# Kernel tuning notes

Measured on AMD Instinct MI355X. Metric: run time of the kernel, lower is better.

The kernel has to match this reference:

```python
import jax, jax.numpy as jnp
import numpy as np

N = 100000      # nodes
E = 3200000     # edges (avg degree 32)
F_IN = 512
F_OUT = 256


def setup_inputs() -> dict:
    key = jax.random.key(0)
    k1, k2, k3, k4, k5, k6 = jax.random.split(key, 6)
    x = jax.random.normal(k1, (N, F_IN), dtype=jnp.float32)
    row = jax.random.randint(k2, (E,), 0, N)            # destination node of each edge
    col = jax.random.randint(k3, (E,), 0, N)            # source node of each edge
    edge_val = jax.random.uniform(k4, (E,), dtype=jnp.float32)  # normalized adj weights
    stdv = 1.0 / np.sqrt(F_OUT)                         # matches reset_parameters()
    weight = jax.random.uniform(k5, (F_IN, F_OUT), dtype=jnp.float32, minval=-stdv, maxval=stdv)
    bias = jax.random.uniform(k6, (F_OUT,), dtype=jnp.float32, minval=-stdv, maxval=stdv)
    return {"input": x, "weight": weight, "bias": bias, "edge_val": edge_val, "row": row, "col": col}


def reference(input, weight, bias, edge_val, row, col):
    # support = X @ W  (dense projection)
    support = input @ weight                             # [N, F_OUT]
    # SpMM: out[r] += a[r,c] * support[c] over COO edges (torch.spmm(adj, support))
    msgs = edge_val[:, None] * support[col]              # [E, F_OUT] gather + scale
    agg = jax.ops.segment_sum(msgs, row, num_segments=input.shape[0])  # scatter-add
    # np.around(..., decimals=3) applied row-wise in the original
    out = jnp.round(agg * 1000.0) / 1000.0
    return out + bias
```

## Files before the change

### kernel.cpp

```cpp
#include <hip/hip_runtime.h>
#include <hip/hip_bf16.h>

#define N_NODES 100000
#define N_EDGES 3200000
#define FIN 512
#define FOUT 256
#define GEMM_BM 128
#define GEMM_BK 32

#define NP 782
#define CAP_LDS 4608
#define SC_CHUNK 16384

typedef __attribute__((ext_vector_type(8))) short short8;
typedef __attribute__((ext_vector_type(4))) float f32x4;

__device__ __forceinline__ unsigned short f2bf(float f) {
    unsigned u = __float_as_uint(f);
    u += 0x7fffu + ((u >> 16) & 1u);
    return (unsigned short)(u >> 16);
}
__device__ __forceinline__ float bf2f(unsigned short h) {
    return __uint_as_float(((unsigned)h) << 16);
}

__global__ __launch_bounds__(256) void prep_weight(const float* __restrict__ W,
                                                   unsigned short* __restrict__ Wt) {
    int idx = blockIdx.x * 256 + threadIdx.x;
    if (idx < FIN * FOUT) {
        int k = idx >> 8;
        int n = idx & 255;
        Wt[(size_t)(k >> 5) * (FOUT * GEMM_BK) + n * GEMM_BK + (k & 31)] = f2bf(W[idx]);
    }
}

__global__ __launch_bounds__(512, 4)
void gemm_kernel(const float* __restrict__ X, const unsigned short* __restrict__ Wt,
                 unsigned short* __restrict__ support) {
    __shared__ unsigned short A_lds[GEMM_BM][40];
    __shared__ unsigned short B_lds[FOUT][40];

    const int t = threadIdx.x;
    const int lane = t & 63;
    const int w = t >> 6;
    const int wm = w >> 2;
    const int wn = w & 3;
    const int q = lane >> 4;
    const int lr = lane & 15;
    const int m0 = blockIdx.x * GEMM_BM;

    f32x4 acc[4][4];
#pragma unroll
    for (int i = 0; i < 4; i++)
#pragma unroll
        for (int j = 0; j < 4; j++) acc[i][j] = (f32x4)0.0f;

    const int arow = t >> 2;
    const int acol = (t & 3) * 8;
    const bool avalid = (m0 + arow) < N_NODES;
    const float* Xp = X + (size_t)(m0 + arow) * FIN + acol;

    const int brow = t >> 1;
    const int bcol = (t & 1) * 16;

    for (int s = 0; s < FIN / GEMM_BK; ++s) {
        union { __hip_bfloat162 h[4]; uint4 v; } pk;
        if (avalid) {
            float4 v0 = *(const float4*)(Xp + s * GEMM_BK);
            float4 v1 = *(const float4*)(Xp + s * GEMM_BK + 4);
            pk.h[0] = __float22bfloat162_rn(make_float2(v0.x, v0.y));
            pk.h[1] = __float22bfloat162_rn(make_float2(v0.z, v0.w));
            pk.h[2] = __float22bfloat162_rn(make_float2(v1.x, v1.y));
            pk.h[3] = __float22bfloat162_rn(make_float2(v1.z, v1.w));
        } else {
            pk.v = make_uint4(0, 0, 0, 0);
        }
        const uint4* bsrc = (const uint4*)(Wt + (size_t)s * (FOUT * GEMM_BK) + brow * GEMM_BK + bcol);
        uint4 b0 = bsrc[0], b1 = bsrc[1];

        __syncthreads();
        *(uint4*)&A_lds[arow][acol] = pk.v;
        *(uint4*)&B_lds[brow][bcol] = b0;
        *(uint4*)&B_lds[brow][bcol + 8] = b1;
        __syncthreads();

        short8 af[4], bfr[4];
#pragma unroll
        for (int i = 0; i < 4; i++) af[i] = *(const short8*)&A_lds[wm * 64 + i * 16 + lr][q * 8];
#pragma unroll
        for (int j = 0; j < 4; j++) bfr[j] = *(const short8*)&B_lds[wn * 64 + j * 16 + lr][q * 8];
#pragma unroll
        for (int i = 0; i < 4; i++)
#pragma unroll
            for (int j = 0; j < 4; j++)
                acc[i][j] = __builtin_amdgcn_mfma_f32_16x16x32_bf16(af[i], bfr[j], acc[i][j], 0, 0, 0);
    }

#pragma unroll
    for (int i = 0; i < 4; i++) {
#pragma unroll
        for (int r = 0; r < 4; r++) {
            int gm = m0 + wm * 64 + i * 16 + q * 4 + r;
            if (gm < N_NODES) {
#pragma unroll
                for (int j = 0; j < 4; j++)
                    support[(size_t)gm * FOUT + wn * 64 + j * 16 + lr] = f2bf(acc[i][j][r]);
            }
        }
    }
}

__global__ __launch_bounds__(256) void part_hist(const int* __restrict__ row,
                                                 unsigned* __restrict__ pcnt) {
    __shared__ unsigned bins[NP];
    for (int i = threadIdx.x; i < NP; i += 256) bins[i] = 0;
    __syncthreads();
    const int e0 = blockIdx.x * 8192;
#pragma unroll
    for (int j = 0; j < 32; ++j) {
        int e = e0 + j * 256 + threadIdx.x;
        if (e < N_EDGES) atomicAdd(&bins[((unsigned)row[e]) >> 7], 1u);
    }
    __syncthreads();
    for (int i = threadIdx.x; i < NP; i += 256)
        if (bins[i]) atomicAdd(&pcnt[i], bins[i]);
}

__global__ __launch_bounds__(1024) void part_scan(const unsigned* __restrict__ pcnt,
                                                  unsigned* __restrict__ base,
                                                  unsigned* __restrict__ cursor,
                                                  unsigned* __restrict__ row_ptr) {
    __shared__ unsigned s[1024];
    const int t = threadIdx.x;
    unsigned v = (t < NP) ? pcnt[t] : 0u;
    s[t] = v;
    __syncthreads();
#pragma unroll
    for (int off = 1; off < 1024; off <<= 1) {
        unsigned tv = (t >= off) ? s[t - off] : 0u;
        __syncthreads();
        s[t] += tv;
        __syncthreads();
    }
    if (t < NP) {
        unsigned b = s[t] - v;
        base[t] = b;
        cursor[t] = b;
    }
    if (t == 0) {
        base[NP] = N_EDGES;
        row_ptr[N_NODES] = N_EDGES;
    }
}

__global__ __launch_bounds__(256) void part_scatter(const int* __restrict__ row,
                                                    const int* __restrict__ col,
                                                    const float* __restrict__ val,
                                                    unsigned* __restrict__ cursor,
                                                    uint2* __restrict__ part) {
    __shared__ unsigned bins[NP];
    __shared__ unsigned gb[NP];
    for (int i = threadIdx.x; i < NP; i += 256) bins[i] = 0;
    __syncthreads();
    const int e0 = blockIdx.x * SC_CHUNK;
#pragma unroll 4
    for (int j = 0; j < SC_CHUNK / 256; ++j) {
        int e = e0 + j * 256 + threadIdx.x;
        if (e < N_EDGES) atomicAdd(&bins[((unsigned)row[e]) >> 7], 1u);
    }
    __syncthreads();
    for (int i = threadIdx.x; i < NP; i += 256) {
        unsigned c = bins[i];
        gb[i] = c ? atomicAdd(&cursor[i], c) : 0u;
        bins[i] = 0;
    }
    __syncthreads();
#pragma unroll 4
    for (int j = 0; j < SC_CHUNK / 256; ++j) {
        int e = e0 + j * 256 + threadIdx.x;
        if (e < N_EDGES) {
            unsigned r = (unsigned)row[e];
            unsigned p = r >> 7;
            unsigned l = atomicAdd(&bins[p], 1u);
            part[gb[p] + l] = make_uint2(((unsigned)col[e]) | ((r & 127u) << 17),
                                         __float_as_uint(val[e]));
        }
    }
}

__global__ __launch_bounds__(256) void part_finalize(const unsigned* __restrict__ base,
                                                     uint2* __restrict__ part,
                                                     unsigned* __restrict__ row_ptr) {
    __shared__ uint2 recs[CAP_LDS];
    __shared__ unsigned ncnt[128], nsc[128], ccur[128];
    const int p = blockIdx.x;
    const int t = threadIdx.x;
    const unsigned b = base[p];
    unsigned cnt = base[p + 1] - b;
    if (cnt > CAP_LDS) cnt = CAP_LDS;
    if (t < 128) ncnt[t] = 0;
    __syncthreads();
    for (unsigned i = t; i < cnt; i += 256) {
        uint2 r = part[b + i];
        recs[i] = r;
        atomicAdd(&ncnt[r.x >> 17], 1u);
    }
    __syncthreads();
    if (t < 128) nsc[t] = ncnt[t];
    __syncthreads();
#pragma unroll
    for (int off = 1; off < 128; off <<= 1) {
        unsigned tv = (t < 128 && t >= off) ? nsc[t - off] : 0u;
        __syncthreads();
        if (t < 128) nsc[t] += tv;
        __syncthreads();
    }
    if (t < 128) {
        unsigned ex = nsc[t] - ncnt[t];
        ccur[t] = ex;
        int node = p * 128 + t;
        if (node < N_NODES) row_ptr[node] = b + ex;
    }
    __syncthreads();
    for (unsigned i = t; i < cnt; i += 256) {
        uint2 r = recs[i];
        unsigned pos = atomicAdd(&ccur[r.x >> 17], 1u);
        part[b + pos] = make_uint2(r.x & 0x1FFFFu, r.y);
    }
}

__global__ __launch_bounds__(256)
void spmm_kernel(const unsigned* __restrict__ row_ptr, const uint2* __restrict__ sorted,
                 const unsigned short* __restrict__ support, const float* __restrict__ bias,
                 float* __restrict__ out) {
    const int lane = threadIdx.x & 63;
    const int n = blockIdx.x * 4 + (threadIdx.x >> 6);
    const unsigned start = __builtin_amdgcn_readfirstlane(row_ptr[n]);
    const unsigned end   = __builtin_amdgcn_readfirstlane(row_ptr[n + 1]);
    const int fo = lane * 4;
    const unsigned short* sp = support + fo;
    float a0 = 0.f, a1 = 0.f, a2 = 0.f, a3 = 0.f;

    unsigned i = start;
    const unsigned nfull = (end - start) >> 3;
    if (nfull) {
        uint2 e[8];
#pragma unroll
        for (int j = 0; j < 8; ++j) e[j] = sorted[i + j];
        for (unsigned bt = 1; bt < nfull; ++bt) {
            ushort4 s[8];
#pragma unroll
            for (int j = 0; j < 8; ++j) s[j] = *(const ushort4*)(sp + (size_t)e[j].x * FOUT);
            uint2 en[8];
#pragma unroll
            for (int j = 0; j < 8; ++j) en[j] = sorted[i + 8 + j];
#pragma unroll
            for (int j = 0; j < 8; ++j) {
                float v = __uint_as_float(e[j].y);
                a0 += v * bf2f(s[j].x); a1 += v * bf2f(s[j].y);
                a2 += v * bf2f(s[j].z); a3 += v * bf2f(s[j].w);
            }
#pragma unroll
            for (int j = 0; j < 8; ++j) e[j] = en[j];
            i += 8;
        }
        ushort4 s[8];
#pragma unroll
        for (int j = 0; j < 8; ++j) s[j] = *(const ushort4*)(sp + (size_t)e[j].x * FOUT);
#pragma unroll
        for (int j = 0; j < 8; ++j) {
            float v = __uint_as_float(e[j].y);
            a0 += v * bf2f(s[j].x); a1 += v * bf2f(s[j].y);
            a2 += v * bf2f(s[j].z); a3 += v * bf2f(s[j].w);
        }
        i += 8;
    }
    for (; i < end; ++i) {
        uint2 e = sorted[i];
        float v = __uint_as_float(e.y);
        ushort4 s0 = *(const ushort4*)(sp + (size_t)e.x * FOUT);
        a0 += v * bf2f(s0.x); a1 += v * bf2f(s0.y); a2 += v * bf2f(s0.z); a3 += v * bf2f(s0.w);
    }

    float4 bv = *(const float4*)(bias + fo);
    float4 r;
    r.x = rintf(a0 * 1000.f) * 0.001f + bv.x;
    r.y = rintf(a1 * 1000.f) * 0.001f + bv.y;
    r.z = rintf(a2 * 1000.f) * 0.001f + bv.z;
    r.w = rintf(a3 * 1000.f) * 0.001f + bv.w;
    *(float4*)(out + (size_t)n * FOUT + fo) = r;
}

extern "C" void kernel_launch(void* const* d_in, const int* in_sizes, int n_in,
                              void* d_out, int out_size, void* d_ws, size_t ws_size,
                              hipStream_t stream) {
    (void)in_sizes; (void)n_in; (void)out_size; (void)ws_size;
    const float* X    = (const float*)d_in[0];
    const float* W    = (const float*)d_in[1];
    const float* bias = (const float*)d_in[2];
    const float* eval = (const float*)d_in[3];
    const int*   row  = (const int*)d_in[4];
    const int*   col  = (const int*)d_in[5];
    float* out = (float*)d_out;

    char* p = (char*)d_ws;
    auto take = [&](size_t bytes) {
        char* r = p;
        p += (bytes + 511) & ~(size_t)511;
        return r;
    };
    unsigned short* support = (unsigned short*)take((size_t)N_NODES * FOUT * 2);
    unsigned short* Wt      = (unsigned short*)take((size_t)FIN * FOUT * 2);
    unsigned*       pcnt    = (unsigned*)take((size_t)NP * 4);
    unsigned*       base    = (unsigned*)take((size_t)(NP + 1) * 4);
    unsigned*       cursor  = (unsigned*)take((size_t)NP * 4);
    unsigned*       row_ptr = (unsigned*)take((size_t)(N_NODES + 1) * 4);
    uint2*          part    = (uint2*)take((size_t)N_EDGES * 8);

    hipMemsetAsync(pcnt, 0, (size_t)NP * 4, stream);
    prep_weight<<<(FIN * FOUT) / 256, 256, 0, stream>>>(W, Wt);
    gemm_kernel<<<(N_NODES + GEMM_BM - 1) / GEMM_BM, 512, 0, stream>>>(X, Wt, support);
    part_hist<<<(N_EDGES + 8191) / 8192, 256, 0, stream>>>(row, pcnt);
    part_scan<<<1, 1024, 0, stream>>>(pcnt, base, cursor, row_ptr);
    part_scatter<<<(N_EDGES + SC_CHUNK - 1) / SC_CHUNK, 256, 0, stream>>>(row, col, eval, cursor, part);
    part_finalize<<<NP, 256, 0, stream>>>(base, part, row_ptr);
    spmm_kernel<<<N_NODES / 4, 256, 0, stream>>>(row_ptr, part, support, bias, out);
}
```

Measured before the change: 718.6 us.

## Split GEMM into N-tiles with direct global-to-LDS swizzled B loads; deepen SpMM batching

The GEMM now launches a 2D grid where each 256-thread block computes a 128x128 output tile. The B operand is pre-swizzled by prep_weight and loaded straight into LDS with global_load_lds, with an XOR swizzle meant to avoid bank conflicts. As a side effect, every X tile is now read and converted to bf16 by two blocks instead of one. The SpMM gather loop is widened from 8 to 16 edges per batch to put more loads in flight, with an extra 8-edge tail path, and the edge buffer is padded to cover the overrun of the prefetch.

```diff
diff --git a/kernel.cpp b/kernel.cpp
--- a/kernel.cpp
+++ b/kernel.cpp
@@ -6,6 +6,7 @@
 #define FIN 512
 #define FOUT 256
 #define GEMM_BM 128
+#define GEMM_BN 128
 #define GEMM_BK 32
 
 #define NP 782
@@ -22,6 +23,12 @@
 }
 __device__ __forceinline__ float bf2f(unsigned short h) {
     return __uint_as_float(((unsigned)h) << 16);
+}
+
+__device__ __forceinline__ void gload_lds16(const void* g, void* l) {
+    __builtin_amdgcn_global_load_lds(
+        (const __attribute__((address_space(1))) unsigned*)g,
+        (__attribute__((address_space(3))) unsigned*)l, 16, 0, 0);
 }
 
 __global__ __launch_bounds__(256) void prep_weight(const float* __restrict__ W,
@@ -30,24 +37,31 @@
     if (idx < FIN * FOUT) {
         int k = idx >> 8;
         int n = idx & 255;
-        Wt[(size_t)(k >> 5) * (FOUT * GEMM_BK) + n * GEMM_BK + (k & 31)] = f2bf(W[idx]);
-    }
-}
-
-__global__ __launch_bounds__(512, 4)
+        int s = k >> 5;
+        int kk = k & 31;
+        int nt = n >> 7;
+        int nl = n & 127;
+        int kb16 = kk >> 3;
+        int u = kb16 ^ (nl & 3) ^ ((nl >> 2) & 3);
+        Wt[(size_t)((s * 2 + nt) << 12) + nl * 32 + u * 8 + (kk & 7)] = f2bf(W[idx]);
+    }
+}
+
+__global__ __launch_bounds__(256)
 void gemm_kernel(const float* __restrict__ X, const unsigned short* __restrict__ Wt,
                  unsigned short* __restrict__ support) {
     __shared__ unsigned short A_lds[GEMM_BM][40];
-    __shared__ unsigned short B_lds[FOUT][40];
+    __shared__ __align__(16) unsigned short bls[4096];
 
     const int t = threadIdx.x;
     const int lane = t & 63;
     const int w = t >> 6;
-    const int wm = w >> 2;
-    const int wn = w & 3;
+    const int wm = w >> 1;
+    const int wn = w & 1;
     const int q = lane >> 4;
     const int lr = lane & 15;
     const int m0 = blockIdx.x * GEMM_BM;
+    const int nt = blockIdx.y;
 
     f32x4 acc[4][4];
 #pragma unroll
@@ -55,40 +69,54 @@
 #pragma unroll
         for (int j = 0; j < 4; j++) acc[i][j] = (f32x4)0.0f;
 
-    const int arow = t >> 2;
-    const int acol = (t & 3) * 8;
+    const int arow = t >> 1;
+    const int acol = (t & 1) * 16;
     const bool avalid = (m0 + arow) < N_NODES;
     const float* Xp = X + (size_t)(m0 + arow) * FIN + acol;
 
-    const int brow = t >> 1;
-    const int bcol = (t & 1) * 16;
+    const unsigned short* gB = Wt + ((size_t)nt << 12) + t * 8;
+    unsigned short* ldsB0 = &bls[w * 512];
+    unsigned short* ldsB1 = &bls[2048 + w * 512];
 
     for (int s = 0; s < FIN / GEMM_BK; ++s) {
-        union { __hip_bfloat162 h[4]; uint4 v; } pk;
+        union { __hip_bfloat162 h[8]; uint4 v[2]; } pk;
         if (avalid) {
             float4 v0 = *(const float4*)(Xp + s * GEMM_BK);
             float4 v1 = *(const float4*)(Xp + s * GEMM_BK + 4);
+            float4 v2 = *(const float4*)(Xp + s * GEMM_BK + 8);
+            float4 v3 = *(const float4*)(Xp + s * GEMM_BK + 12);
             pk.h[0] = __float22bfloat162_rn(make_float2(v0.x, v0.y));
             pk.h[1] = __float22bfloat162_rn(make_float2(v0.z, v0.w));
             pk.h[2] = __float22bfloat162_rn(make_float2(v1.x, v1.y));
             pk.h[3] = __float22bfloat162_rn(make_float2(v1.z, v1.w));
+            pk.h[4] = __float22bfloat162_rn(make_float2(v2.x, v2.y));
+            pk.h[5] = __float22bfloat162_rn(make_float2(v2.z, v2.w));
+            pk.h[6] = __float22bfloat162_rn(make_float2(v3.x, v3.y));
+            pk.h[7] = __float22bfloat162_rn(make_float2(v3.z, v3.w));
         } else {
-            pk.v = make_uint4(0, 0, 0, 0);
-        }
-        const uint4* bsrc = (const uint4*)(Wt + (size_t)s * (FOUT * GEMM_BK) + brow * GEMM_BK + bcol);
-        uint4 b0 = bsrc[0], b1 = bsrc[1];
-
-        __syncthreads();
-        *(uint4*)&A_lds[arow][acol] = pk.v;
-        *(uint4*)&B_lds[brow][bcol] = b0;
-        *(uint4*)&B_lds[brow][bcol + 8] = b1;
+            pk.v[0] = make_uint4(0, 0, 0, 0);
+            pk.v[1] = make_uint4(0, 0, 0, 0);
+        }
+
+        __syncthreads();
+
+        gload_lds16(gB + (size_t)s * 8192, ldsB0);
+        gload_lds16(gB + (size_t)s * 8192 + 2048, ldsB1);
+
+        *(uint4*)&A_lds[arow][acol] = pk.v[0];
+        *(uint4*)&A_lds[arow][acol + 8] = pk.v[1];
+
         __syncthreads();
 
         short8 af[4], bfr[4];
 #pragma unroll
         for (int i = 0; i < 4; i++) af[i] = *(const short8*)&A_lds[wm * 64 + i * 16 + lr][q * 8];
 #pragma unroll
-        for (int j = 0; j < 4; j++) bfr[j] = *(const short8*)&B_lds[wn * 64 + j * 16 + lr][q * 8];
+        for (int j = 0; j < 4; j++) {
+            int nl = wn * 64 + j * 16 + lr;
+            int u = q ^ (nl & 3) ^ ((nl >> 2) & 3);
+            bfr[j] = *(const short8*)&bls[nl * 32 + u * 8];
+        }
 #pragma unroll
         for (int i = 0; i < 4; i++)
 #pragma unroll
@@ -96,6 +124,7 @@
                 acc[i][j] = __builtin_amdgcn_mfma_f32_16x16x32_bf16(af[i], bfr[j], acc[i][j], 0, 0, 0);
     }
 
+    const int n0 = nt * GEMM_BN;
 #pragma unroll
     for (int i = 0; i < 4; i++) {
 #pragma unroll
@@ -104,7 +133,7 @@
             if (gm < N_NODES) {
 #pragma unroll
                 for (int j = 0; j < 4; j++)
-                    support[(size_t)gm * FOUT + wn * 64 + j * 16 + lr] = f2bf(acc[i][j][r]);
+                    support[(size_t)gm * FOUT + n0 + wn * 64 + j * 16 + lr] = f2bf(acc[i][j][r]);
             }
         }
     }
@@ -242,28 +271,43 @@
     float a0 = 0.f, a1 = 0.f, a2 = 0.f, a3 = 0.f;
 
     unsigned i = start;
-    const unsigned nfull = (end - start) >> 3;
+    const unsigned nfull = (end - start) >> 4;
     if (nfull) {
-        uint2 e[8];
-#pragma unroll
-        for (int j = 0; j < 8; ++j) e[j] = sorted[i + j];
+        uint2 e[16];
+#pragma unroll
+        for (int j = 0; j < 16; ++j) e[j] = sorted[i + j];
         for (unsigned bt = 1; bt < nfull; ++bt) {
-            ushort4 s[8];
-#pragma unroll
-            for (int j = 0; j < 8; ++j) s[j] = *(const ushort4*)(sp + (size_t)e[j].x * FOUT);
-            uint2 en[8];
-#pragma unroll
-            for (int j = 0; j < 8; ++j) en[j] = sorted[i + 8 + j];
-#pragma unroll
-            for (int j = 0; j < 8; ++j) {
+            ushort4 s[16];
+#pragma unroll
+            for (int j = 0; j < 16; ++j) s[j] = *(const ushort4*)(sp + (size_t)e[j].x * FOUT);
+            uint2 en[16];
+#pragma unroll
+            for (int j = 0; j < 16; ++j) en[j] = sorted[i + 16 + j];
+#pragma unroll
+            for (int j = 0; j < 16; ++j) {
                 float v = __uint_as_float(e[j].y);
                 a0 += v * bf2f(s[j].x); a1 += v * bf2f(s[j].y);
                 a2 += v * bf2f(s[j].z); a3 += v * bf2f(s[j].w);
             }
 #pragma unroll
-            for (int j = 0; j < 8; ++j) e[j] = en[j];
-            i += 8;
-        }
+            for (int j = 0; j < 16; ++j) e[j] = en[j];
+            i += 16;
+        }
+        ushort4 s[16];
+#pragma unroll
+        for (int j = 0; j < 16; ++j) s[j] = *(const ushort4*)(sp + (size_t)e[j].x * FOUT);
+#pragma unroll
+        for (int j = 0; j < 16; ++j) {
+            float v = __uint_as_float(e[j].y);
+            a0 += v * bf2f(s[j].x); a1 += v * bf2f(s[j].y);
+            a2 += v * bf2f(s[j].z); a3 += v * bf2f(s[j].w);
+        }
+        i += 16;
+    }
+    if (end - i >= 8) {
+        uint2 e[8];
+#pragma unroll
+        for (int j = 0; j < 8; ++j) e[j] = sorted[i + j];
         ushort4 s[8];
 #pragma unroll
         for (int j = 0; j < 8; ++j) s[j] = *(const ushort4*)(sp + (size_t)e[j].x * FOUT);
@@ -315,11 +359,11 @@
     unsigned*       base    = (unsigned*)take((size_t)(NP + 1) * 4);
     unsigned*       cursor  = (unsigned*)take((size_t)NP * 4);
     unsigned*       row_ptr = (unsigned*)take((size_t)(N_NODES + 1) * 4);
-    uint2*          part    = (uint2*)take((size_t)N_EDGES * 8);
+    uint2*          part    = (uint2*)take((size_t)N_EDGES * 8 + 1024);
 
     hipMemsetAsync(pcnt, 0, (size_t)NP * 4, stream);
     prep_weight<<<(FIN * FOUT) / 256, 256, 0, stream>>>(W, Wt);
-    gemm_kernel<<<(N_NODES + GEMM_BM - 1) / GEMM_BM, 512, 0, stream>>>(X, Wt, support);
+    gemm_kernel<<<dim3((N_NODES + GEMM_BM - 1) / GEMM_BM, FOUT / GEMM_BN), 256, 0, stream>>>(X, Wt, support);
     part_hist<<<(N_EDGES + 8191) / 8192, 256, 0, stream>>>(row, pcnt);
     part_scan<<<1, 1024, 0, stream>>>(pcnt, base, cursor, row_ptr);
     part_scatter<<<(N_EDGES + SC_CHUNK - 1) / SC_CHUNK, 256, 0, stream>>>(row, col, eval, cursor, part);
```

Result: slower. 760.0 us (+5.8%).
